# Optimization experiments

Hardware: AMD Instinct MI355X
Metric: run time of the kernel (lower is better)

Reference implementation:

```python
import jax, jax.numpy as jnp
import numpy as np

B, L_IN, D = 4, 4096, 1024
R_MIN, R_MAX = 0.9, 0.999


def setup_inputs() -> dict:
    key = jax.random.key(0)
    k0, k1, k2 = jax.random.split(key, 3)
    inputs = jax.random.normal(k0, (B, L_IN, D), jnp.float32)
    Wi = jax.random.normal(k1, (2 * D, D), jnp.float32) / np.sqrt(D)
    bi = jnp.zeros((2 * D,), jnp.float32)
    Wo = jax.random.normal(k2, (D, 2 * D), jnp.float32) / np.sqrt(2 * D)
    bo = jnp.zeros((D,), jnp.float32)
    # LRU stable-ring initialization, exactly as in the torch module
    rng = np.random.default_rng(0)
    u1 = rng.random(D)
    u2 = rng.random(D)
    v_log = np.log(-0.5 * np.log(u1 * (R_MAX ** 2 - R_MIN ** 2) + R_MIN ** 2))
    theta_log = np.log(u2 * np.pi * 2)
    gamma_log = np.log(np.sqrt(1.0 - np.exp(-np.exp(v_log)) ** 2))
    params_log = jnp.asarray(np.stack([v_log, theta_log, gamma_log]), jnp.float32)
    return {"inputs": inputs, "Wi": Wi, "bi": bi, "Wo": Wo, "bo": bo,
            "params_log": params_log}


def _lru_forward(inputs, Wi, bi, Wo, bo, params_log):
    b, l_in, d = inputs.shape
    u = inputs @ Wi.T + bi                      # [B, L, 2D]
    v, theta, gamma = jnp.exp(params_log)       # each [D]
    # torch.view_as_complex: interleaved (real, imag) pairs along last dim
    uc = u.reshape(b, l_in, d, 2)
    x = jax.lax.complex(uc[..., 0], uc[..., 1])  # [B, L, D] complex64
    log2_L = int(np.ceil(np.log2(l_in)))
    L = 2 ** log2_L
    x = jnp.pad(x, ((0, 0), (0, L - l_in), (0, 0)))
    # Blelloch-style log-depth scan: x_t = lambda * x_{t-1} + u_t,
    # lambda = exp(-v + i*theta)
    for i in range(1, log2_L + 1):
        blk = 2 ** i
        xb = x.reshape(b * L // blk, blk, d)
        x1, x2 = xb[:, : blk // 2], xb[:, blk // 2:]
        pos = jnp.arange(1, blk // 2 + 1, dtype=jnp.float32)  # [blk/2]
        lambs = jnp.exp(jax.lax.complex(-pos[:, None] * v,
                                        pos[:, None] * theta))  # [blk/2, D]
        x2 = x2 + lambs * x1[:, -1:]
        x = jnp.concatenate([x1, x2], axis=1).reshape(b, L, d)
    x = x[:, :l_in] * gamma.astype(x.dtype)     # normalize, drop padding
    xr = jnp.concatenate([x.real, x.imag], axis=-1)  # [B, L, 2D]
    out = xr @ Wo.T + bo
    return jax.nn.relu(out)


def reference(inputs, Wi, bi, Wo, bo, params_log):
    return _lru_forward(inputs, Wi, bi, Wo, bo, params_log)
```

## Files before the change

kernel.cpp:

```cpp
#include <hip/hip_runtime.h>

#define BB 4
#define LL 4096
#define DD 1024
#define SS 64
#define TT 64

typedef __attribute__((ext_vector_type(4))) float  floatx4;
typedef __attribute__((ext_vector_type(8))) short  shortx8;

static __device__ __forceinline__ unsigned short f2bf(float f) {
    unsigned int u = __float_as_uint(f);
    u += 0x7fffu + ((u >> 16) & 1u);
    return (unsigned short)(u >> 16);
}
static __device__ __forceinline__ float bf2f(unsigned short h) {
    return __uint_as_float(((unsigned int)h) << 16);
}

__global__ void cast_bf16_kernel(const float4* __restrict__ src,
                                 ushort4* __restrict__ dst, int n4) {
    int i = blockIdx.x * blockDim.x + threadIdx.x;
    if (i < n4) {
        float4 v = src[i];
        ushort4 o;
        o.x = f2bf(v.x); o.y = f2bf(v.y); o.z = f2bf(v.z); o.w = f2bf(v.w);
        dst[i] = o;
    }
}

template<int K, int NT, int EPI>
__global__ __launch_bounds__(256)
void gemm_bt(const unsigned short* __restrict__ A,
             const unsigned short* __restrict__ B,
             const float* __restrict__ bias,
             void* __restrict__ Cp) {
    constexpr int N = NT * 128;
    __shared__ __align__(16) short As[128 * 32];
    __shared__ __align__(16) short Bs[128 * 32];

    const int tid = threadIdx.x;
    const int b   = blockIdx.x;
    const int xcd = b & 7;
    const int i2  = b >> 3;
    const int tileM = ((i2 / NT) * 8 + xcd) * 128;
    const int tileN = (i2 % NT) * 128;

    const int lane  = tid & 63;
    const int wave  = tid >> 6;
    const int wm    = (wave >> 1) * 64;
    const int wn    = (wave & 1) * 64;
    const int r16   = lane & 15;
    const int quad  = lane >> 4;

    floatx4 acc[4][4] = {};

    const int q0 = tid, q1 = tid + 256;
    const int ra0 = q0 >> 2, ca0 = ((q0 & 3) ^ ((ra0 >> 1) & 3)) * 8;
    const int ra1 = q1 >> 2, ca1 = ((q1 & 3) ^ ((ra1 >> 1) & 3)) * 8;
    short* As0 = &As[(q0 & ~63) * 8];
    short* As1 = &As[(q1 & ~63) * 8];
    short* Bs0 = &Bs[(q0 & ~63) * 8];
    short* Bs1 = &Bs[(q1 & ~63) * 8];

    const int fsw = (quad ^ ((r16 >> 1) & 3)) * 8;

    for (int k0 = 0; k0 < K; k0 += 32) {
        __builtin_amdgcn_global_load_lds(
            (const __attribute__((address_space(1))) void*)&A[(size_t)(tileM + ra0) * K + k0 + ca0],
            (__attribute__((address_space(3))) void*)As0, 16, 0, 0);
        __builtin_amdgcn_global_load_lds(
            (const __attribute__((address_space(1))) void*)&A[(size_t)(tileM + ra1) * K + k0 + ca1],
            (__attribute__((address_space(3))) void*)As1, 16, 0, 0);
        __builtin_amdgcn_global_load_lds(
            (const __attribute__((address_space(1))) void*)&B[(size_t)(tileN + ra0) * K + k0 + ca0],
            (__attribute__((address_space(3))) void*)Bs0, 16, 0, 0);
        __builtin_amdgcn_global_load_lds(
            (const __attribute__((address_space(1))) void*)&B[(size_t)(tileN + ra1) * K + k0 + ca1],
            (__attribute__((address_space(3))) void*)Bs1, 16, 0, 0);
        __syncthreads();

        shortx8 af[4], bfv[4];
#pragma unroll
        for (int i = 0; i < 4; ++i)
            af[i] = *(const shortx8*)(&As[(wm + i * 16 + r16) * 32 + fsw]);
#pragma unroll
        for (int j = 0; j < 4; ++j)
            bfv[j] = *(const shortx8*)(&Bs[(wn + j * 16 + r16) * 32 + fsw]);
#pragma unroll
        for (int i = 0; i < 4; ++i)
#pragma unroll
            for (int j = 0; j < 4; ++j)
                acc[i][j] = __builtin_amdgcn_mfma_f32_16x16x32_bf16(
                    af[i], bfv[j], acc[i][j], 0, 0, 0);
        __syncthreads();
    }

#pragma unroll
    for (int i = 0; i < 4; ++i) {
#pragma unroll
        for (int j = 0; j < 4; ++j) {
            const int col = tileN + wn + j * 16 + r16;
            const float bv = bias[col];
#pragma unroll
            for (int r = 0; r < 4; ++r) {
                const int row = tileM + wm + i * 16 + quad * 4 + r;
                float v = acc[i][j][r] + bv;
                if (EPI == 0) {
                    ((unsigned short*)Cp)[(size_t)row * N + col] = f2bf(v);
                } else {
                    ((float*)Cp)[(size_t)row * N + col] = fmaxf(v, 0.0f);
                }
            }
        }
    }
}

__global__ __launch_bounds__(256)
void scanA(const unsigned short* __restrict__ u,
           const float* __restrict__ plog,
           float2* __restrict__ Eend) {
    const int d = blockIdx.x * 256 + threadIdx.x;
    const int c = blockIdx.y, b = blockIdx.z;
    const float v  = expf(plog[d]);
    const float th = expf(plog[DD + d]);
    const float a  = expf(-v);
    const float lr = a * cosf(th), li = a * sinf(th);
    float zr = 0.f, zi = 0.f;
    const unsigned short* up = u + (size_t)(b * LL + c * TT) * (2 * DD) + 2 * d;
#pragma unroll 8
    for (int tl = 0; tl < TT; ++tl) {
        unsigned int pair = *(const unsigned int*)up;
        float xr_ = bf2f((unsigned short)(pair & 0xffffu));
        float xi_ = bf2f((unsigned short)(pair >> 16));
        float nzr = lr * zr - li * zi + xr_;
        float nzi = lr * zi + li * zr + xi_;
        zr = nzr; zi = nzi;
        up += 2 * DD;
    }
    Eend[(size_t)c * (BB * DD) + b * DD + d] = make_float2(zr, zi);
}

__global__ __launch_bounds__(256)
void scanC(const unsigned short* __restrict__ u,
           const float* __restrict__ plog,
           const float2* __restrict__ Eend,
           unsigned short* __restrict__ xr) {
    const int d = blockIdx.x * 256 + threadIdx.x;
    const int c = blockIdx.y, b = blockIdx.z;
    const float v  = expf(plog[d]);
    const float th = expf(plog[DD + d]);
    const float g  = expf(plog[2 * DD + d]);
    const float a  = expf(-v);
    const float lr = a * cosf(th), li = a * sinf(th);

    const float aT = expf(-(float)TT * v);
    const float Lr = aT * cosf((float)TT * th), Li = aT * sinf((float)TT * th);
    float yr = 0.f, yi = 0.f;
    for (int cc = 0; cc < c; ++cc) {
        float2 e = Eend[(size_t)cc * (BB * DD) + b * DD + d];
        float nyr = Lr * yr - Li * yi + e.x;
        float nyi = Lr * yi + Li * yr + e.y;
        yr = nyr; yi = nyi;
    }

    const unsigned short* up = u + (size_t)(b * LL + c * TT) * (2 * DD) + 2 * d;
    unsigned short* xp = xr + (size_t)(b * LL + c * TT) * (2 * DD) + d;
#pragma unroll 4
    for (int tl = 0; tl < TT; ++tl) {
        unsigned int pair = *(const unsigned int*)up;
        float xr_ = bf2f((unsigned short)(pair & 0xffffu));
        float xi_ = bf2f((unsigned short)(pair >> 16));
        float nyr = lr * yr - li * yi + xr_;
        float nyi = lr * yi + li * yr + xi_;
        yr = nyr; yi = nyi;
        xp[0]  = f2bf(g * yr);
        xp[DD] = f2bf(g * yi);
        up += 2 * DD;
        xp += 2 * DD;
    }
}

extern "C" void kernel_launch(void* const* d_in, const int* in_sizes, int n_in,
                              void* d_out, int out_size, void* d_ws, size_t ws_size,
                              hipStream_t stream) {
    const float* inputs = (const float*)d_in[0];
    const float* Wi     = (const float*)d_in[1];
    const float* bi     = (const float*)d_in[2];
    const float* Wo     = (const float*)d_in[3];
    const float* bo     = (const float*)d_in[4];
    const float* plog   = (const float*)d_in[5];
    float* out = (float*)d_out;

    const size_t M = (size_t)BB * LL;
    unsigned short* u_bf  = (unsigned short*)d_ws;
    unsigned short* xr_bf = u_bf  + M * 2 * DD;
    unsigned short* in_bf = xr_bf + M * 2 * DD;
    unsigned short* Wi_bf = in_bf + M * DD;
    unsigned short* Wo_bf = Wi_bf + (size_t)2 * DD * DD;
    float2* Eend = (float2*)(Wo_bf + (size_t)2 * DD * DD);

    {
        int n4 = (int)(M * DD / 4);
        cast_bf16_kernel<<<(n4 + 255) / 256, 256, 0, stream>>>(
            (const float4*)inputs, (ushort4*)in_bf, n4);
        int w4 = (int)(2 * DD * DD / 4);
        cast_bf16_kernel<<<(w4 + 255) / 256, 256, 0, stream>>>(
            (const float4*)Wi, (ushort4*)Wi_bf, w4);
        cast_bf16_kernel<<<(w4 + 255) / 256, 256, 0, stream>>>(
            (const float4*)Wo, (ushort4*)Wo_bf, w4);
    }

    gemm_bt<DD, 16, 0><<<(M / 128) * 16, 256, 0, stream>>>(
        in_bf, Wi_bf, bi, (void*)u_bf);

    scanA<<<dim3(DD / 256, SS, BB), 256, 0, stream>>>(u_bf, plog, Eend);
    scanC<<<dim3(DD / 256, SS, BB), 256, 0, stream>>>(u_bf, plog, Eend, xr_bf);

    gemm_bt<2 * DD, 8, 1><<<(M / 128) * 8, 256, 0, stream>>>(
        xr_bf, Wo_bf, bo, (void*)out);
}
```

Measured before the change: 351.6 us.

## Use 32x32 MFMA in GEMMs, fuse cast kernels, vectorize scans over two channels

The GEMM inner loop moves from 16x16x32 to 32x32x16 bf16 MFMA tiles, cutting LDS fragment reads per MFMA and changing the accumulator layout and epilogue row mapping. The three bf16 cast launches are merged into one kernel to save launch overhead. The scan kernels now handle two channels per thread with wider loads and packed stores, halving the grid but improving memory access width. Risks include the epilogue's strided scalar stores and fewer threads in the scan stages.

```diff
diff --git a/kernel.cpp b/kernel.cpp
--- a/kernel.cpp
+++ b/kernel.cpp
@@ -6,8 +6,8 @@
 #define SS 64
 #define TT 64
 
-typedef __attribute__((ext_vector_type(4))) float  floatx4;
-typedef __attribute__((ext_vector_type(8))) short  shortx8;
+typedef __attribute__((ext_vector_type(16))) float  floatx16;
+typedef __attribute__((ext_vector_type(8)))  short  shortx8;
 
 static __device__ __forceinline__ unsigned short f2bf(float f) {
     unsigned int u = __float_as_uint(f);
@@ -18,15 +18,20 @@
     return __uint_as_float(((unsigned int)h) << 16);
 }
 
-__global__ void cast_bf16_kernel(const float4* __restrict__ src,
-                                 ushort4* __restrict__ dst, int n4) {
+#define NIN4 (BB * LL * DD / 4)
+#define NW4  (2 * DD * DD / 4)
+__global__ void cast_all_kernel(const float4* __restrict__ s_in, ushort4* __restrict__ d_inb,
+                                const float4* __restrict__ s_wi, ushort4* __restrict__ d_wib,
+                                const float4* __restrict__ s_wo, ushort4* __restrict__ d_wob) {
     int i = blockIdx.x * blockDim.x + threadIdx.x;
-    if (i < n4) {
-        float4 v = src[i];
-        ushort4 o;
-        o.x = f2bf(v.x); o.y = f2bf(v.y); o.z = f2bf(v.z); o.w = f2bf(v.w);
-        dst[i] = o;
-    }
+    const float4* s; ushort4* d; int j;
+    if (i < NIN4)                 { s = s_in; d = d_inb; j = i; }
+    else if (i < NIN4 + NW4)      { s = s_wi; d = d_wib; j = i - NIN4; }
+    else                          { s = s_wo; d = d_wob; j = i - NIN4 - NW4; }
+    float4 v = s[j];
+    ushort4 o;
+    o.x = f2bf(v.x); o.y = f2bf(v.y); o.z = f2bf(v.z); o.w = f2bf(v.w);
+    d[j] = o;
 }
 
 template<int K, int NT, int EPI>
@@ -46,14 +51,14 @@
     const int tileM = ((i2 / NT) * 8 + xcd) * 128;
     const int tileN = (i2 % NT) * 128;
 
-    const int lane  = tid & 63;
-    const int wave  = tid >> 6;
-    const int wm    = (wave >> 1) * 64;
-    const int wn    = (wave & 1) * 64;
-    const int r16   = lane & 15;
-    const int quad  = lane >> 4;
-
-    floatx4 acc[4][4] = {};
+    const int lane = tid & 63;
+    const int wave = tid >> 6;
+    const int wm   = (wave >> 1) * 64;
+    const int wn   = (wave & 1) * 64;
+    const int r32  = lane & 31;
+    const int ks   = lane >> 5;
+
+    floatx16 acc[2][2] = {};
 
     const int q0 = tid, q1 = tid + 256;
     const int ra0 = q0 >> 2, ca0 = ((q0 & 3) ^ ((ra0 >> 1) & 3)) * 8;
@@ -63,8 +68,6 @@
     short* Bs0 = &Bs[(q0 & ~63) * 8];
     short* Bs1 = &Bs[(q1 & ~63) * 8];
 
-    const int fsw = (quad ^ ((r16 >> 1) & 3)) * 8;
-
     for (int k0 = 0; k0 < K; k0 += 32) {
         __builtin_amdgcn_global_load_lds(
             (const __attribute__((address_space(1))) void*)&A[(size_t)(tileM + ra0) * K + k0 + ca0],
@@ -80,31 +83,43 @@
             (__attribute__((address_space(3))) void*)Bs1, 16, 0, 0);
         __syncthreads();
 
-        shortx8 af[4], bfv[4];
-#pragma unroll
-        for (int i = 0; i < 4; ++i)
-            af[i] = *(const shortx8*)(&As[(wm + i * 16 + r16) * 32 + fsw]);
-#pragma unroll
-        for (int j = 0; j < 4; ++j)
-            bfv[j] = *(const shortx8*)(&Bs[(wn + j * 16 + r16) * 32 + fsw]);
-#pragma unroll
-        for (int i = 0; i < 4; ++i)
-#pragma unroll
-            for (int j = 0; j < 4; ++j)
-                acc[i][j] = __builtin_amdgcn_mfma_f32_16x16x32_bf16(
-                    af[i], bfv[j], acc[i][j], 0, 0, 0);
+        shortx8 af[2][2], bfr[2][2];
+#pragma unroll
+        for (int i = 0; i < 2; ++i) {
+            const int row = wm + i * 32 + r32;
+            const int sw  = (row >> 1) & 3;
+#pragma unroll
+            for (int kc = 0; kc < 2; ++kc)
+                af[i][kc] = *(const shortx8*)(&As[row * 32 + ((kc * 2 + ks) ^ sw) * 8]);
+        }
+#pragma unroll
+        for (int j = 0; j < 2; ++j) {
+            const int row = wn + j * 32 + r32;
+            const int sw  = (row >> 1) & 3;
+#pragma unroll
+            for (int kc = 0; kc < 2; ++kc)
+                bfr[j][kc] = *(const shortx8*)(&Bs[row * 32 + ((kc * 2 + ks) ^ sw) * 8]);
+        }
+#pragma unroll
+        for (int kc = 0; kc < 2; ++kc)
+#pragma unroll
+            for (int i = 0; i < 2; ++i)
+#pragma unroll
+                for (int j = 0; j < 2; ++j)
+                    acc[i][j] = __builtin_amdgcn_mfma_f32_32x32x16_bf16(
+                        af[i][kc], bfr[j][kc], acc[i][j], 0, 0, 0);
         __syncthreads();
     }
 
 #pragma unroll
-    for (int i = 0; i < 4; ++i) {
-#pragma unroll
-        for (int j = 0; j < 4; ++j) {
-            const int col = tileN + wn + j * 16 + r16;
+    for (int i = 0; i < 2; ++i) {
+#pragma unroll
+        for (int j = 0; j < 2; ++j) {
+            const int col = tileN + wn + j * 32 + r32;
             const float bv = bias[col];
 #pragma unroll
-            for (int r = 0; r < 4; ++r) {
-                const int row = tileM + wm + i * 16 + quad * 4 + r;
+            for (int r = 0; r < 16; ++r) {
+                const int row = tileM + wm + i * 32 + (r & 3) + 8 * (r >> 2) + 4 * ks;
                 float v = acc[i][j][r] + bv;
                 if (EPI == 0) {
                     ((unsigned short*)Cp)[(size_t)row * N + col] = f2bf(v);
@@ -120,25 +135,29 @@
 void scanA(const unsigned short* __restrict__ u,
            const float* __restrict__ plog,
            float2* __restrict__ Eend) {
-    const int d = blockIdx.x * 256 + threadIdx.x;
+    const int d0 = (blockIdx.x * 256 + threadIdx.x) * 2;
     const int c = blockIdx.y, b = blockIdx.z;
-    const float v  = expf(plog[d]);
-    const float th = expf(plog[DD + d]);
-    const float a  = expf(-v);
-    const float lr = a * cosf(th), li = a * sinf(th);
-    float zr = 0.f, zi = 0.f;
-    const unsigned short* up = u + (size_t)(b * LL + c * TT) * (2 * DD) + 2 * d;
-#pragma unroll 8
+    const float v0  = expf(plog[d0]),      v1  = expf(plog[d0 + 1]);
+    const float th0 = expf(plog[DD + d0]), th1 = expf(plog[DD + d0 + 1]);
+    const float a0 = expf(-v0), a1 = expf(-v1);
+    const float lr0 = a0 * cosf(th0), li0 = a0 * sinf(th0);
+    const float lr1 = a1 * cosf(th1), li1 = a1 * sinf(th1);
+    float zr0 = 0.f, zi0 = 0.f, zr1 = 0.f, zi1 = 0.f;
+    const unsigned short* up = u + (size_t)(b * LL + c * TT) * (2 * DD) + 2 * d0;
+#pragma unroll 4
     for (int tl = 0; tl < TT; ++tl) {
-        unsigned int pair = *(const unsigned int*)up;
-        float xr_ = bf2f((unsigned short)(pair & 0xffffu));
-        float xi_ = bf2f((unsigned short)(pair >> 16));
-        float nzr = lr * zr - li * zi + xr_;
-        float nzi = lr * zi + li * zr + xi_;
-        zr = nzr; zi = nzi;
+        uint2 pr = *(const uint2*)up;
+        float xr0 = bf2f((unsigned short)(pr.x & 0xffffu));
+        float xi0 = bf2f((unsigned short)(pr.x >> 16));
+        float xr1 = bf2f((unsigned short)(pr.y & 0xffffu));
+        float xi1 = bf2f((unsigned short)(pr.y >> 16));
+        float t;
+        t = lr0 * zr0 - li0 * zi0 + xr0; zi0 = lr0 * zi0 + li0 * zr0 + xi0; zr0 = t;
+        t = lr1 * zr1 - li1 * zi1 + xr1; zi1 = lr1 * zi1 + li1 * zr1 + xi1; zr1 = t;
         up += 2 * DD;
     }
-    Eend[(size_t)c * (BB * DD) + b * DD + d] = make_float2(zr, zi);
+    *(float4*)&Eend[(size_t)c * (BB * DD) + b * DD + d0] =
+        make_float4(zr0, zi0, zr1, zi1);
 }
 
 __global__ __launch_bounds__(256)
@@ -146,36 +165,42 @@
            const float* __restrict__ plog,
            const float2* __restrict__ Eend,
            unsigned short* __restrict__ xr) {
-    const int d = blockIdx.x * 256 + threadIdx.x;
+    const int d0 = (blockIdx.x * 256 + threadIdx.x) * 2;
     const int c = blockIdx.y, b = blockIdx.z;
-    const float v  = expf(plog[d]);
-    const float th = expf(plog[DD + d]);
-    const float g  = expf(plog[2 * DD + d]);
-    const float a  = expf(-v);
-    const float lr = a * cosf(th), li = a * sinf(th);
-
-    const float aT = expf(-(float)TT * v);
-    const float Lr = aT * cosf((float)TT * th), Li = aT * sinf((float)TT * th);
-    float yr = 0.f, yi = 0.f;
+    const float v0  = expf(plog[d0]),      v1  = expf(plog[d0 + 1]);
+    const float th0 = expf(plog[DD + d0]), th1 = expf(plog[DD + d0 + 1]);
+    const float g0  = expf(plog[2 * DD + d0]), g1 = expf(plog[2 * DD + d0 + 1]);
+    const float a0 = expf(-v0), a1 = expf(-v1);
+    const float lr0 = a0 * cosf(th0), li0 = a0 * sinf(th0);
+    const float lr1 = a1 * cosf(th1), li1 = a1 * sinf(th1);
+
+    const float aT0 = expf(-(float)TT * v0), aT1 = expf(-(float)TT * v1);
+    const float Lr0 = aT0 * cosf((float)TT * th0), Li0 = aT0 * sinf((float)TT * th0);
+    const float Lr1 = aT1 * cosf((float)TT * th1), Li1 = aT1 * sinf((float)TT * th1);
+    float yr0 = 0.f, yi0 = 0.f, yr1 = 0.f, yi1 = 0.f;
     for (int cc = 0; cc < c; ++cc) {
-        float2 e = Eend[(size_t)cc * (BB * DD) + b * DD + d];
-        float nyr = Lr * yr - Li * yi + e.x;
-        float nyi = Lr * yi + Li * yr + e.y;
-        yr = nyr; yi = nyi;
-    }
-
-    const unsigned short* up = u + (size_t)(b * LL + c * TT) * (2 * DD) + 2 * d;
-    unsigned short* xp = xr + (size_t)(b * LL + c * TT) * (2 * DD) + d;
+        float4 e = *(const float4*)&Eend[(size_t)cc * (BB * DD) + b * DD + d0];
+        float t;
+        t = Lr0 * yr0 - Li0 * yi0 + e.x; yi0 = Lr0 * yi0 + Li0 * yr0 + e.y; yr0 = t;
+        t = Lr1 * yr1 - Li1 * yi1 + e.z; yi1 = Lr1 * yi1 + Li1 * yr1 + e.w; yr1 = t;
+    }
+
+    const unsigned short* up = u + (size_t)(b * LL + c * TT) * (2 * DD) + 2 * d0;
+    unsigned short* xp = xr + (size_t)(b * LL + c * TT) * (2 * DD) + d0;
 #pragma unroll 4
     for (int tl = 0; tl < TT; ++tl) {
-        unsigned int pair = *(const unsigned int*)up;
-        float xr_ = bf2f((unsigned short)(pair & 0xffffu));
-        float xi_ = bf2f((unsigned short)(pair >> 16));
-        float nyr = lr * yr - li * yi + xr_;
-        float nyi = lr * yi + li * yr + xi_;
-        yr = nyr; yi = nyi;
-        xp[0]  = f2bf(g * yr);
-        xp[DD] = f2bf(g * yi);
+        uint2 pr = *(const uint2*)up;
+        float xr0 = bf2f((unsigned short)(pr.x & 0xffffu));
+        float xi0 = bf2f((unsigned short)(pr.x >> 16));
+        float xr1 = bf2f((unsigned short)(pr.y & 0xffffu));
+        float xi1 = bf2f((unsigned short)(pr.y >> 16));
+        float t;
+        t = lr0 * yr0 - li0 * yi0 + xr0; yi0 = lr0 * yi0 + li0 * yr0 + xi0; yr0 = t;
+        t = lr1 * yr1 - li1 * yi1 + xr1; yi1 = lr1 * yi1 + li1 * yr1 + xi1; yr1 = t;
+        *(unsigned int*)&xp[0]  = (unsigned int)f2bf(g0 * yr0) |
+                                  ((unsigned int)f2bf(g1 * yr1) << 16);
+        *(unsigned int*)&xp[DD] = (unsigned int)f2bf(g0 * yi0) |
+                                  ((unsigned int)f2bf(g1 * yi1) << 16);
         up += 2 * DD;
         xp += 2 * DD;
     }
@@ -201,21 +226,18 @@
     float2* Eend = (float2*)(Wo_bf + (size_t)2 * DD * DD);
 
     {
-        int n4 = (int)(M * DD / 4);
-        cast_bf16_kernel<<<(n4 + 255) / 256, 256, 0, stream>>>(
-            (const float4*)inputs, (ushort4*)in_bf, n4);
-        int w4 = (int)(2 * DD * DD / 4);
-        cast_bf16_kernel<<<(w4 + 255) / 256, 256, 0, stream>>>(
-            (const float4*)Wi, (ushort4*)Wi_bf, w4);
-        cast_bf16_kernel<<<(w4 + 255) / 256, 256, 0, stream>>>(
-            (const float4*)Wo, (ushort4*)Wo_bf, w4);
+        int total4 = NIN4 + 2 * NW4;
+        cast_all_kernel<<<total4 / 256, 256, 0, stream>>>(
+            (const float4*)inputs, (ushort4*)in_bf,
+            (const float4*)Wi,     (ushort4*)Wi_bf,
+            (const float4*)Wo,     (ushort4*)Wo_bf);
     }
 
     gemm_bt<DD, 16, 0><<<(M / 128) * 16, 256, 0, stream>>>(
         in_bf, Wi_bf, bi, (void*)u_bf);
 
-    scanA<<<dim3(DD / 256, SS, BB), 256, 0, stream>>>(u_bf, plog, Eend);
-    scanC<<<dim3(DD / 256, SS, BB), 256, 0, stream>>>(u_bf, plog, Eend, xr_bf);
+    scanA<<<dim3(DD / 512, SS, BB), 256, 0, stream>>>(u_bf, plog, Eend);
+    scanC<<<dim3(DD / 512, SS, BB), 256, 0, stream>>>(u_bf, plog, Eend, xr_bf);
 
     gemm_bt<2 * DD, 8, 1><<<(M / 128) * 8, 256, 0, stream>>>(
         xr_bf, Wo_bf, bo, (void*)out);
```

Result: no change. 353.7 us (+0.6%).
